# Kernel optimization log

Measured on AMD Instinct MI355X. Metric: run time of the kernel, lower is better.

Reference implementation:

```python
import jax, jax.numpy as jnp
import numpy as np

N_HEADS = 8
D_HEAD = 64
SCALE = D_HEAD ** -0.5


def setup_inputs() -> dict:
    key = jax.random.key(0)
    k1, k2, k3 = jax.random.split(key, 3)
    B, H, W, C = 16, 32, 32, 512
    ft = jax.random.normal(k1, (B, H, W, C), dtype=jnp.float32)
    # Dense layers: to_qkv -> n_heads*n_dim_heads*3 = 1536 units, to_out -> n_channels
    w_qkv = jax.random.normal(k2, (C, N_HEADS * D_HEAD * 3), dtype=jnp.float32) * (C ** -0.5)
    b_qkv = jnp.zeros((N_HEADS * D_HEAD * 3,), dtype=jnp.float32)
    w_out = jax.random.normal(k3, (N_HEADS * D_HEAD, C), dtype=jnp.float32) * ((N_HEADS * D_HEAD) ** -0.5)
    b_out = jnp.zeros((C,), dtype=jnp.float32)
    return {"ft": ft, "w_qkv": w_qkv, "b_qkv": b_qkv, "w_out": w_out, "b_out": b_out}


def reference(ft, w_qkv, b_qkv, w_out, b_out):
    B, H, W, C = ft.shape
    N = H * W
    x = ft.reshape(B, N, C)                       # b (h w) c
    qkv = x @ w_qkv + b_qkv                       # b n (heads * 3*d_head)
    qkv = qkv.reshape(B, N, N_HEADS, 3 * D_HEAD)  # 'b x (h d) -> b x h d'
    q, k, v = jnp.split(qkv, 3, axis=-1)          # each: b n heads d_head
    attn = jnp.einsum('bxhd,byhd->bxyh', q, k) * SCALE
    attn = jax.nn.softmax(attn, axis=2)           # softmax over key axis y
    res = jnp.einsum('bxyh,byhd->bxhd', attn, v)  # b x h d
    res = res.reshape(B, N, N_HEADS * D_HEAD)     # 'b x h d -> b x (h d)'
    res = res @ w_out + b_out
    res = res + x                                 # residual with pre-qkv flattened input
    return res.reshape(B, H, W, C)
```

## Files before the change

### kernel.cpp

```cpp
#include <hip/hip_runtime.h>
#include <hip/hip_bf16.h>

using u16 = unsigned short;
using u32 = unsigned int;
typedef __attribute__((ext_vector_type(8))) short short8;
typedef __attribute__((ext_vector_type(4))) float f32x4;

#define MFMA16(A, B, C) __builtin_amdgcn_mfma_f32_16x16x32_bf16((A), (B), (C), 0, 0, 0)

__device__ __forceinline__ u16 f2bf(float f) {
  union { float f; u32 i; } v; v.f = f;
  u32 x = v.i;
  return (u16)((x + 0x7fffu + ((x >> 16) & 1u)) >> 16);
}
__device__ __forceinline__ u32 pkbf(float a, float b) {
  union { __hip_bfloat162 h; u32 u; } v;
  v.h = __float22bfloat162_rn(make_float2(a, b));
  return v.u;
}
__device__ __forceinline__ u32 cvtpk(float a, float b) {
  u32 r;
  asm("v_cvt_pk_bf16_f32 %0, %1, %2" : "=v"(r) : "v"(a), "v"(b));
  return r;
}
__device__ __forceinline__ void gl16(const u16* g, u16* l) {
  __builtin_amdgcn_global_load_lds(
      (const __attribute__((address_space(1))) u32*)g,
      (__attribute__((address_space(3))) u32*)l, 16, 0, 0);
}

__global__ __launch_bounds__(256) void conv_x(const float* __restrict__ X,
                                              u16* __restrict__ Xbf) {
  const int i = (blockIdx.x * 256 + threadIdx.x) * 8;
  float4 a = *(const float4*)(X + i);
  float4 b = *(const float4*)(X + i + 4);
  uint4 o;
  o.x = pkbf(a.x, a.y); o.y = pkbf(a.z, a.w);
  o.z = pkbf(b.x, b.y); o.w = pkbf(b.z, b.w);
  *(uint4*)(Xbf + i) = o;
}

__global__ __launch_bounds__(256) void transpose_w(
    const float* __restrict__ Wq, const float* __restrict__ Wo,
    u16* __restrict__ Wqt, u16* __restrict__ Wot) {
  const int z = blockIdx.z;
  if (z == 1 && blockIdx.x >= 16) return;
  const float* src = z ? Wo : Wq;
  u16* dst = z ? Wot : Wqt;
  const int ncols = z ? 512 : 1536;
  __shared__ float tile[32][33];
  const int t = threadIdx.x;
  const int kt = blockIdx.y * 32, nt = blockIdx.x * 32;
  const int r = t >> 3, c4 = (t & 7) * 4;
  float4 v = *(const float4*)(src + (size_t)(kt + r) * ncols + nt + c4);
  tile[r][c4 + 0] = v.x; tile[r][c4 + 1] = v.y;
  tile[r][c4 + 2] = v.z; tile[r][c4 + 3] = v.w;
  __syncthreads();
  uint2 p = make_uint2(pkbf(tile[c4 + 0][r], tile[c4 + 1][r]),
                       pkbf(tile[c4 + 2][r], tile[c4 + 3][r]));
  *(uint2*)(dst + (size_t)(nt + r) * 512 + kt + c4) = p;
}

__global__ __launch_bounds__(512) void qkv_gemm(
    const u16* __restrict__ Xbf, const u16* __restrict__ Wt,
    const float* __restrict__ Bias,
    u16* __restrict__ Qp, u16* __restrict__ Kp, u16* __restrict__ Vt) {
  __shared__ u16 SM[36864];
  #define XS(b, r) (&SM[(b) * 4096 + (r) * 32])
  #define WS(b, r) (&SM[12288 + (b) * 8192 + (r) * 32])
  #define ES(r, c) SM[(r) * 264 + (c)]
  const int t = threadIdx.x;
  const int lid = blockIdx.y * 6 + blockIdx.x;
  const int sid = (lid & 7) * 96 + (lid >> 3);
  const int bm = (sid / 6) * 128, bn = (sid % 6) * 256;
  const int w = t >> 6, lane = t & 63, quad = lane >> 4, l16 = lane & 15;
  const int mtb = (w >> 2) * 64, ntb = (w & 3) * 64;
  const int rr = lane >> 2;
  const int gch = ((lane & 3) ^ ((lane >> 3) & 3)) * 8;
  const int sw = (quad ^ ((l16 >> 1) & 3)) * 8;

  const u16* xg0 = Xbf + (size_t)(bm + w * 16 + rr) * 512 + gch;
  const u16* wg0 = Wt + (size_t)(bn + w * 16 + rr) * 512 + gch;
  const u16* wg1 = wg0 + (size_t)128 * 512;

  f32x4 acc[4][4];
  const f32x4 z4 = {0.f, 0.f, 0.f, 0.f};
  #pragma unroll
  for (int mi = 0; mi < 4; mi++)
    #pragma unroll
    for (int ni = 0; ni < 4; ni++) acc[mi][ni] = z4;

  gl16(xg0, XS(0, w * 16));
  gl16(wg0, WS(0, w * 16)); gl16(wg1, WS(0, w * 16 + 128));
  gl16(xg0 + 32, XS(1, w * 16));
  gl16(wg0 + 32, WS(1, w * 16)); gl16(wg1 + 32, WS(1, w * 16 + 128));
  asm volatile("s_waitcnt vmcnt(3)" ::: "memory");
  __builtin_amdgcn_s_barrier();

  for (int k = 0; k < 16; ++k) {
    const int cur = k % 3;
    if (k < 14) {
      const int nx2 = (k + 2) % 3;
      const int kn = (k + 2) * 32;
      gl16(xg0 + kn, XS(nx2, w * 16));
      gl16(wg0 + kn, WS(nx2, w * 16));
      gl16(wg1 + kn, WS(nx2, w * 16 + 128));
    }
    short8 af[4], bf4[4];
    #pragma unroll
    for (int mi = 0; mi < 4; mi++)
      af[mi] = *(const short8*)(XS(cur, mtb + mi * 16 + l16) + sw);
    #pragma unroll
    for (int ni = 0; ni < 4; ni++)
      bf4[ni] = *(const short8*)(WS(cur, ntb + ni * 16 + l16) + sw);
    #pragma unroll
    for (int mi = 0; mi < 4; mi++)
      #pragma unroll
      for (int ni = 0; ni < 4; ni++)
        acc[mi][ni] = MFMA16(af[mi], bf4[ni], acc[mi][ni]);
    if (k < 15) {
      if (k < 14) asm volatile("s_waitcnt vmcnt(3) lgkmcnt(0)" ::: "memory");
      else        asm volatile("s_waitcnt vmcnt(0) lgkmcnt(0)" ::: "memory");
      __builtin_amdgcn_s_barrier();
    }
  }

  __syncthreads();
  #pragma unroll
  for (int ni = 0; ni < 4; ni++) {
    const int g = bn + ntb + ni * 16;
    const int h = g / 192, rm = g % 192;
    const int type = rm >> 6, dbase = rm & 63;
    const float bias = Bias[g + l16];
    const float qsc = (type == 0) ? 0.125f * 1.44269504088896340736f : 1.0f;
    #pragma unroll
    for (int mi = 0; mi < 4; mi++) {
      if (type == 2) {
        const int row0 = bm + mtb + mi * 16 + quad * 4;
        const int b = row0 >> 10, n0 = row0 & 1023;
        const size_t bh = (size_t)(b * 8 + h) * 65536;
        uint2 p = make_uint2(pkbf(acc[mi][ni][0] + bias, acc[mi][ni][1] + bias),
                             pkbf(acc[mi][ni][2] + bias, acc[mi][ni][3] + bias));
        *(uint2*)(Vt + bh + (size_t)(dbase + l16) * 1024 + n0) = p;
      } else {
        const int lrow = mtb + mi * 16 + quad * 4;
        const int lcol = ntb + ni * 16 + l16;
        #pragma unroll
        for (int r = 0; r < 4; r++)
          ES(lrow + r, lcol) = f2bf((acc[mi][ni][r] + bias) * qsc);
      }
    }
  }
  __syncthreads();
  #pragma unroll
  for (int rep = 0; rep < 8; rep++) {
    const int row = rep * 16 + (t >> 5);
    const int ch = t & 31;
    const int g = bn + ch * 8;
    const int rm = g % 192;
    const int type = rm >> 6;
    if (type < 2) {
      const int h = g / 192;
      const int row0 = bm + row;
      const int b = row0 >> 10, n0 = row0 & 1023;
      uint4 v = *(const uint4*)&ES(row, ch * 8);
      u16* dst = (type ? Kp : Qp) + (size_t)(b * 8 + h) * 65536 +
                 (size_t)n0 * 64 + (rm & 63);
      *(uint4*)dst = v;
    }
  }
  #undef XS
  #undef WS
  #undef ES
}

__global__ __launch_bounds__(512, 4) void attn_mfma(
    const u16* __restrict__ Qp, const u16* __restrict__ Kp,
    const u16* __restrict__ Vt, u16* __restrict__ ATT) {
  __shared__ u16 Ks[2][64][64];
  __shared__ u16 Vs[2][64][64];
  const int t = threadIdx.x, w = t >> 6, lane = t & 63;
  const int quad = lane >> 4, l16 = lane & 15;
  const int bx = blockIdx.x;
  const int c = bx & 7, g = bx >> 3;
  const int qt = g & 3, u = g >> 2;
  const int bh_id = u * 8 + c;
  const int b = bh_id >> 3, h = bh_id & 7;
  const size_t bh = (size_t)bh_id * 65536;
  const u16* Qb = Qp + bh;
  const u16* Kb = Kp + bh;
  const u16* Vb = Vt + bh;
  const int q0 = qt * 256 + w * 32;

  const u16* kg = Kb + (size_t)(t >> 3) * 64 + ((t & 7) ^ ((t >> 3) & 7)) * 8;
  const u16* vg = Vb + (size_t)(t >> 3) * 1024 + ((t & 7) ^ ((t >> 3) & 7)) * 8;
  u16* ks0 = &Ks[0][0][0] + w * 512;
  u16* ks1 = &Ks[1][0][0] + w * 512;
  u16* vs0 = &Vs[0][0][0] + w * 512;
  u16* vs1 = &Vs[1][0][0] + w * 512;

  const int m7 = l16 & 7;
  const char* ksb = (const char*)&Ks[0][0][0];
  const char* vsb = (const char*)&Vs[0][0][0];
  const int kb0 = l16 * 128 + (quad ^ m7) * 16;
  const int kb1 = kb0 ^ 64;
  int vo[2];
  #pragma unroll
  for (int ks = 0; ks < 2; ks++)
    vo[ks] = l16 * 128 + ((4 * ks + quad) ^ m7) * 16;

  short8 qfA[2], qfB[2];
  #pragma unroll
  for (int ks = 0; ks < 2; ks++) {
    qfA[ks] = *(const short8*)(Qb + (size_t)(q0 + l16) * 64 + ks * 32 + quad * 8);
    qfB[ks] = *(const short8*)(Qb + (size_t)(q0 + 16 + l16) * 64 + ks * 32 + quad * 8);
  }

  const short8 vone = {(short)0x3F80, (short)0x3F80, (short)0x3F80,
                       (short)0x3F80, (short)0x3F80, (short)0x3F80,
                       (short)0x3F80, (short)0x3F80};

  f32x4 OfA[4], OfB[4], OlA, OlB;
  const f32x4 z4 = {0.f, 0.f, 0.f, 0.f};
  #pragma unroll
  for (int ni = 0; ni < 4; ni++) { OfA[ni] = z4; OfB[ni] = z4; }
  OlA = z4; OlB = z4;

  gl16(kg, ks0);
  gl16(vg, vs0);
  __syncthreads();

  for (int kt = 0; kt < 16; ++kt) {
    const int cur = kt & 1;
    if (kt < 15) {
      gl16(kg + (kt + 1) * 4096, cur ? ks0 : ks1);
      gl16(vg + (kt + 1) * 64,   cur ? vs0 : vs1);
    }
    const int co = cur << 13;

    u32 eA[4], oA[4], eB[4], oB[4];
    #pragma unroll
    for (int nt = 0; nt < 4; nt++) {
      short8 k0f = *(const short8*)(ksb + co + kb0 + nt * 2048);
      short8 k1f = *(const short8*)(ksb + co + kb1 + nt * 2048);
      f32x4 sA = z4, sB = z4;
      sA = MFMA16(k0f, qfA[0], sA);
      sB = MFMA16(k0f, qfB[0], sB);
      sA = MFMA16(k1f, qfA[1], sA);
      sB = MFMA16(k1f, qfB[1], sB);
      float a0 = __builtin_amdgcn_exp2f(sA[0]);
      float a1 = __builtin_amdgcn_exp2f(sA[1]);
      float a2 = __builtin_amdgcn_exp2f(sA[2]);
      float a3 = __builtin_amdgcn_exp2f(sA[3]);
      float b0 = __builtin_amdgcn_exp2f(sB[0]);
      float b1 = __builtin_amdgcn_exp2f(sB[1]);
      float b2 = __builtin_amdgcn_exp2f(sB[2]);
      float b3 = __builtin_amdgcn_exp2f(sB[3]);
      const u32 loA = cvtpk(a0, a1), hiA = cvtpk(a2, a3);
      const u32 loB = cvtpk(b0, b1), hiB = cvtpk(b2, b3);
      if (nt & 1) {
        oA[(nt >> 1) * 2] = loA; oA[(nt >> 1) * 2 + 1] = hiA;
        oB[(nt >> 1) * 2] = loB; oB[(nt >> 1) * 2 + 1] = hiB;
      } else {
        eA[(nt >> 1) * 2] = loA; eA[(nt >> 1) * 2 + 1] = hiA;
        eB[(nt >> 1) * 2] = loB; eB[(nt >> 1) * 2 + 1] = hiB;
      }
    }
    #pragma unroll
    for (int i = 0; i < 4; i++) {
      auto tA = __builtin_amdgcn_permlane32_swap(eA[i], oA[i], false, false);
      auto xA = __builtin_amdgcn_permlane16_swap(tA[0], tA[1], false, false);
      eA[i] = xA[0]; oA[i] = xA[1];
      auto tB = __builtin_amdgcn_permlane32_swap(eB[i], oB[i], false, false);
      auto xB = __builtin_amdgcn_permlane16_swap(tB[0], tB[1], false, false);
      eB[i] = xB[0]; oB[i] = xB[1];
    }
    #pragma unroll
    for (int ks = 0; ks < 2; ks++) {
      union { short8 v; u32 u[4]; } paA, paB;
      paA.u[0] = eA[2 * ks]; paA.u[1] = eA[2 * ks + 1];
      paA.u[2] = oA[2 * ks]; paA.u[3] = oA[2 * ks + 1];
      paB.u[0] = eB[2 * ks]; paB.u[1] = eB[2 * ks + 1];
      paB.u[2] = oB[2 * ks]; paB.u[3] = oB[2 * ks + 1];
      #pragma unroll
      for (int ni = 0; ni < 4; ni++) {
        short8 vf = *(const short8*)(vsb + co + vo[ks] + ni * 2048);
        OfA[ni] = MFMA16(paA.v, vf, OfA[ni]);
        OfB[ni] = MFMA16(paB.v, vf, OfB[ni]);
      }
      OlA = MFMA16(paA.v, vone, OlA);
      OlB = MFMA16(paB.v, vone, OlB);
    }
    __syncthreads();
  }
  #pragma unroll
  for (int r = 0; r < 4; r++) {
    const float invA = 1.0f / OlA[r];
    const float invB = 1.0f / OlB[r];
    const int rowA = b * 1024 + q0 + quad * 4 + r;
    const int rowB = rowA + 16;
    #pragma unroll
    for (int ni = 0; ni < 4; ni++) {
      ATT[(size_t)rowA * 512 + h * 64 + ni * 16 + l16] = f2bf(OfA[ni][r] * invA);
      ATT[(size_t)rowB * 512 + h * 64 + ni * 16 + l16] = f2bf(OfB[ni][r] * invB);
    }
  }
}

__global__ __launch_bounds__(512) void out_proj(
    const u16* __restrict__ A, const u16* __restrict__ Wt,
    const float* __restrict__ Bias, const float* __restrict__ FT,
    float* __restrict__ OUT) {
  __shared__ u16 As[3][128][32];
  __shared__ u16 Ws[3][128][32];
  const int t = threadIdx.x;
  const int lid = blockIdx.y * 4 + blockIdx.x;
  const int sid = (lid & 7) * 64 + (lid >> 3);
  const int bm = (sid / 4) * 128, bn = (sid % 4) * 128;
  const int w = t >> 6, lane = t & 63, quad = lane >> 4, l16 = lane & 15;
  const int mtb = (w >> 1) * 32, ntb = (w & 1) * 64;
  const int rr = lane >> 2;
  const int gch = ((lane & 3) ^ ((lane >> 3) & 3)) * 8;
  const int sw = (quad ^ ((l16 >> 1) & 3)) * 8;

  const u16* ag = A + (size_t)(bm + w * 16 + rr) * 512 + gch;
  const u16* wg = Wt + (size_t)(bn + w * 16 + rr) * 512 + gch;

  f32x4 acc[2][4];
  const f32x4 z4 = {0.f, 0.f, 0.f, 0.f};
  #pragma unroll
  for (int mi = 0; mi < 2; mi++)
    #pragma unroll
    for (int ni = 0; ni < 4; ni++) acc[mi][ni] = z4;

  gl16(ag, &As[0][w * 16][0]);      gl16(wg, &Ws[0][w * 16][0]);
  gl16(ag + 32, &As[1][w * 16][0]); gl16(wg + 32, &Ws[1][w * 16][0]);
  asm volatile("s_waitcnt vmcnt(2)" ::: "memory");
  __builtin_amdgcn_s_barrier();

  for (int k = 0; k < 16; ++k) {
    const int cur = k % 3;
    if (k < 14) {
      const int nx2 = (k + 2) % 3;
      const int kn = (k + 2) * 32;
      gl16(ag + kn, &As[nx2][w * 16][0]);
      gl16(wg + kn, &Ws[nx2][w * 16][0]);
    }
    short8 af[2], bf4[4];
    #pragma unroll
    for (int mi = 0; mi < 2; mi++)
      af[mi] = *(const short8*)&As[cur][mtb + mi * 16 + l16][sw];
    #pragma unroll
    for (int ni = 0; ni < 4; ni++)
      bf4[ni] = *(const short8*)&Ws[cur][ntb + ni * 16 + l16][sw];
    #pragma unroll
    for (int mi = 0; mi < 2; mi++)
      #pragma unroll
      for (int ni = 0; ni < 4; ni++)
        acc[mi][ni] = MFMA16(af[mi], bf4[ni], acc[mi][ni]);
    if (k < 15) {
      if (k < 14) asm volatile("s_waitcnt vmcnt(2) lgkmcnt(0)" ::: "memory");
      else        asm volatile("s_waitcnt vmcnt(0) lgkmcnt(0)" ::: "memory");
      __builtin_amdgcn_s_barrier();
    }
  }

  #pragma unroll
  for (int ni = 0; ni < 4; ni++) {
    const int g = bn + ntb + ni * 16;
    const float bias = Bias[g + l16];
    #pragma unroll
    for (int mi = 0; mi < 2; mi++) {
      const int row0 = bm + mtb + mi * 16 + quad * 4;
      #pragma unroll
      for (int r = 0; r < 4; r++) {
        const size_t idx = (size_t)(row0 + r) * 512 + g + l16;
        OUT[idx] = acc[mi][ni][r] + bias + FT[idx];
      }
    }
  }
}

extern "C" void kernel_launch(void* const* d_in, const int* in_sizes, int n_in,
                              void* d_out, int out_size, void* d_ws, size_t ws_size,
                              hipStream_t stream) {
  const float* ft    = (const float*)d_in[0];
  const float* w_qkv = (const float*)d_in[1];
  const float* b_qkv = (const float*)d_in[2];
  const float* w_out = (const float*)d_in[3];
  const float* b_out = (const float*)d_in[4];
  float* out = (float*)d_out;

  char* p = (char*)d_ws;
  u16* Xbf    = (u16*)(p);
  u16* ATT    = Xbf;
  u16* Wqkv_t = (u16*)(p + 16777216);
  u16* Wout_t = (u16*)(p + 18350080);
  u16* Qp     = (u16*)(p + 18874368);
  u16* Kp     = (u16*)(p + 35651584);
  u16* Vt     = (u16*)(p + 52428800);

  conv_x     <<<4096, 256, 0, stream>>>(ft, Xbf);
  transpose_w<<<dim3(48, 16, 2), 256, 0, stream>>>(w_qkv, w_out, Wqkv_t, Wout_t);
  qkv_gemm   <<<dim3(6, 128), 512, 0, stream>>>(Xbf, Wqkv_t, b_qkv, Qp, Kp, Vt);
  attn_mfma  <<<dim3(512), 512, 0, stream>>>(Qp, Kp, Vt, ATT);
  out_proj   <<<dim3(4, 128), 512, 0, stream>>>(ATT, Wout_t, b_out, ft, out);
}
```

Baseline: 185.3 us.

## Triple-buffer K/V tiles in attention with prefetch distance two and manual waitcnt

Moves the attention kernel's K/V shared-memory staging from double to triple buffering, prefetching two tiles ahead. The full __syncthreads is replaced by an explicit s_waitcnt that leaves the newest loads in flight, followed by a raw barrier. It also raises wave priority around the PV MFMA section. The aim is to hide global load latency better and remove a full drain each iteration, at the cost of 50% more LDS per block, which may reduce occupancy at 4 blocks per CU.

After: 182.4 us. Within noise of the previous version (-1.6%).

```diff
diff --git a/kernel.cpp b/kernel.cpp
--- a/kernel.cpp
+++ b/kernel.cpp
@@ -177,8 +177,8 @@
 __global__ __launch_bounds__(512, 4) void attn_mfma(
     const u16* __restrict__ Qp, const u16* __restrict__ Kp,
     const u16* __restrict__ Vt, u16* __restrict__ ATT) {
-  __shared__ u16 Ks[2][64][64];
-  __shared__ u16 Vs[2][64][64];
+  __shared__ u16 Ks[3][64][64];
+  __shared__ u16 Vs[3][64][64];
   const int t = threadIdx.x, w = t >> 6, lane = t & 63;
   const int quad = lane >> 4, l16 = lane & 15;
   const int bx = blockIdx.x;
@@ -194,10 +194,8 @@
 
   const u16* kg = Kb + (size_t)(t >> 3) * 64 + ((t & 7) ^ ((t >> 3) & 7)) * 8;
   const u16* vg = Vb + (size_t)(t >> 3) * 1024 + ((t & 7) ^ ((t >> 3) & 7)) * 8;
-  u16* ks0 = &Ks[0][0][0] + w * 512;
-  u16* ks1 = &Ks[1][0][0] + w * 512;
-  u16* vs0 = &Vs[0][0][0] + w * 512;
-  u16* vs1 = &Vs[1][0][0] + w * 512;
+  u16* ksW = &Ks[0][0][0] + w * 512;
+  u16* vsW = &Vs[0][0][0] + w * 512;
 
   const int m7 = l16 & 7;
   const char* ksb = (const char*)&Ks[0][0][0];
@@ -226,17 +224,18 @@
   for (int ni = 0; ni < 4; ni++) { OfA[ni] = z4; OfB[ni] = z4; }
   OlA = z4; OlB = z4;
 
-  gl16(kg, ks0);
-  gl16(vg, vs0);
-  __syncthreads();
-
+  gl16(kg, ksW);               gl16(vg, vsW);
+  gl16(kg + 4096, ksW + 4096); gl16(vg + 64, vsW + 4096);
+  asm volatile("s_waitcnt vmcnt(2)" ::: "memory");
+  __builtin_amdgcn_s_barrier();
+
+  int c3 = 0, n3 = 2;
   for (int kt = 0; kt < 16; ++kt) {
-    const int cur = kt & 1;
-    if (kt < 15) {
-      gl16(kg + (kt + 1) * 4096, cur ? ks0 : ks1);
-      gl16(vg + (kt + 1) * 64,   cur ? vs0 : vs1);
-    }
-    const int co = cur << 13;
+    if (kt < 14) {
+      gl16(kg + (kt + 2) * 4096, ksW + n3 * 4096);
+      gl16(vg + (kt + 2) * 64,   vsW + n3 * 4096);
+    }
+    const int co = c3 * 8192;
 
     u32 eA[4], oA[4], eB[4], oB[4];
     #pragma unroll
@@ -275,6 +274,7 @@
       auto xB = __builtin_amdgcn_permlane16_swap(tB[0], tB[1], false, false);
       eB[i] = xB[0]; oB[i] = xB[1];
     }
+    __builtin_amdgcn_s_setprio(1);
     #pragma unroll
     for (int ks = 0; ks < 2; ks++) {
       union { short8 v; u32 u[4]; } paA, paB;
@@ -291,7 +291,14 @@
       OlA = MFMA16(paA.v, vone, OlA);
       OlB = MFMA16(paB.v, vone, OlB);
     }
-    __syncthreads();
+    __builtin_amdgcn_s_setprio(0);
+    if (kt < 15) {
+      if (kt < 14) asm volatile("s_waitcnt vmcnt(2) lgkmcnt(0)" ::: "memory");
+      else         asm volatile("s_waitcnt vmcnt(0) lgkmcnt(0)" ::: "memory");
+      __builtin_amdgcn_s_barrier();
+    }
+    c3 = (c3 == 2) ? 0 : c3 + 1;
+    n3 = (n3 == 2) ? 0 : n3 + 1;
   }
   #pragma unroll
   for (int r = 0; r < 4; r++) {
```
